# Kernel tuning notes

Measured on AMD Instinct MI355X. Metric: run time of the kernel, lower is better.

The kernel has to match this reference:

```python
import jax, jax.numpy as jnp
import numpy as np

B, H, W, C = 4, 64, 64, 512
EPS = 1e-3  # keras BatchNormalization default epsilon


def setup_inputs() -> dict:
    key = jax.random.key(0)
    ks = jax.random.split(key, 16)
    c8, c2 = C // 8, C // 2
    sc = lambda fan_in: 1.0 / np.sqrt(fan_in)
    inp = {
        "x": jax.random.normal(ks[0], (B, H, W, C), dtype=jnp.float32),
        # 1x1 conv weights as [Cin, Cout] matrices
        "wf": jax.random.normal(ks[1], (C, c8), dtype=jnp.float32) * sc(C),
        "bf": jnp.zeros((c8,), jnp.float32),
        "wg": jax.random.normal(ks[2], (C, c8), dtype=jnp.float32) * sc(C),
        "bg": jnp.zeros((c8,), jnp.float32),
        "wh": jax.random.normal(ks[3], (C, c2), dtype=jnp.float32) * sc(C),
        "bh": jnp.zeros((c2,), jnp.float32),
        "wo": jax.random.normal(ks[4], (c2, C), dtype=jnp.float32) * sc(c2),
        "bo": jnp.zeros((C,), jnp.float32),
        "gamma": jax.random.normal(ks[5], (1,), dtype=jnp.float32) * 0.05,
        # concat 1x1 conv (2C -> C), has bias (use_batchnorm=False default)
        "wc": jax.random.normal(ks[6], (2 * C, C), dtype=jnp.float32) * sc(2 * C),
        "bc": jnp.zeros((C,), jnp.float32),
        # BN inference params (moving statistics)
        "bn_scale": jnp.ones((C,), jnp.float32),
        "bn_bias": jnp.zeros((C,), jnp.float32),
        "bn_mean": jnp.zeros((C,), jnp.float32),
        "bn_var": jnp.ones((C,), jnp.float32),
    }
    return inp


def reference(x, wf, bf, wg, bg, wh, bh, wo, bo, gamma, wc, bc,
              bn_scale, bn_bias, bn_mean, bn_var):
    b, h, w, c = x.shape
    n = h * w
    xf = x.reshape(b, n, c)
    f = xf @ wf + bf          # [B, N, C/8]
    g = xf @ wg + bg          # [B, N, C/8]
    hv = xf @ wh + bh         # [B, N, C/2]
    s = jnp.einsum('bnd,bmd->bnm', g, f)   # [B, N, N]
    beta = jax.nn.softmax(s, axis=-1)
    o = jnp.einsum('bnm,bmd->bnd', beta, hv)  # [B, N, C/2]
    o = o @ wo + bo                            # [B, N, C]
    att = gamma * o + xf                       # gamma-scaled residual
    cat = jnp.concatenate([att, xf], axis=-1)  # [B, N, 2C]
    y = cat @ wc + bc
    # BatchNorm inference + relu
    y = (y - bn_mean) * (bn_scale / jnp.sqrt(bn_var + EPS)) + bn_bias
    y = jax.nn.relu(y)
    return y.reshape(b, h, w, c)
```

## Files before the change

kernel.cpp:

```cpp
#include <hip/hip_runtime.h>
#include <hip/hip_bf16.h>

typedef __bf16 bf16x8 __attribute__((ext_vector_type(8)));
typedef float f32x4 __attribute__((ext_vector_type(4)));

#define EPSBN 1e-3f

constexpr int NPIX = 4096;
constexpr int D2 = 256;

#define RAW_BARRIER() do { \
  asm volatile("s_waitcnt lgkmcnt(0)" ::: "memory"); \
  __builtin_amdgcn_s_barrier(); \
  asm volatile("" ::: "memory"); \
} while (0)

__global__ __launch_bounds__(256) void k_cvt(const float* __restrict__ x,
                                             __bf16* __restrict__ xb, int n4) {
  int i = blockIdx.x * 256 + threadIdx.x;
  if (i >= n4) return;
  float4 v = reinterpret_cast<const float4*>(x)[i];
  union { __bf16 h[4]; uint2 u; } o;
  o.h[0] = (__bf16)v.x; o.h[1] = (__bf16)v.y; o.h[2] = (__bf16)v.z; o.h[3] = (__bf16)v.w;
  reinterpret_cast<uint2*>(xb)[i] = o.u;
}

__global__ __launch_bounds__(256) void kp_wfgh(const float* __restrict__ wf,
                                               const float* __restrict__ wg,
                                               const float* __restrict__ wh,
                                               __bf16* __restrict__ WT) {
  int idx = blockIdx.x * 256 + threadIdx.x;
  int c = idx >> 9, k = idx & 511;
  float v = (c < 64) ? wf[k * 64 + c] : (c < 128) ? wg[k * 64 + (c - 64)] : wh[k * 256 + (c - 128)];
  WT[idx] = (__bf16)v;
}

__global__ __launch_bounds__(128) void kp_bias384(const float* bf_, const float* bg_,
                                                  const float* bh_, float* bias) {
  int c = blockIdx.x * 128 + threadIdx.x;
  bias[c] = (c < 64) ? bf_[c] : (c < 128) ? bg_[c - 64] : bh_[c - 128];
}

__global__ __launch_bounds__(256) void kp_wow(const float* __restrict__ wo,
                                              const float* __restrict__ wc,
                                              float* __restrict__ Wow) {
  int idx = blockIdx.x * 256 + threadIdx.x;
  int d = idx >> 9, c = idx & 511;
  float acc = 0.f;
  for (int j = 0; j < 512; ++j) acc += wo[d * 512 + j] * wc[j * 512 + c];
  Wow[idx] = acc;
}

__global__ __launch_bounds__(256) void kp_wcat(const float* __restrict__ Wow,
                                               const float* __restrict__ wc,
                                               const float* __restrict__ gamma,
                                               const float* __restrict__ bns,
                                               const float* __restrict__ bnv,
                                               __bf16* __restrict__ WT) {
  int idx = blockIdx.x * 256 + threadIdx.x;
  int c = idx / 768, k = idx % 768;
  float s = bns[c] * rsqrtf(bnv[c] + EPSBN);
  float v;
  if (k < 256) v = gamma[0] * Wow[k * 512 + c] * s;
  else { int kk = k - 256; v = (wc[kk * 512 + c] + wc[(512 + kk) * 512 + c]) * s; }
  WT[idx] = (__bf16)v;
}

__global__ __launch_bounds__(256) void kp_biasF(const float* bo, const float* wc, const float* bc,
                                                const float* gamma, const float* bns, const float* bnb,
                                                const float* bnm, const float* bnv, float* biasF) {
  int c = blockIdx.x * 256 + threadIdx.x;
  float s = bns[c] * rsqrtf(bnv[c] + EPSBN);
  float acc = 0.f;
  for (int j = 0; j < 512; ++j) acc += bo[j] * wc[j * 512 + c];
  float pre = bc[c] + gamma[0] * acc;
  biasF[c] = (pre - bnm[c]) * s + bnb[c];
}

template <int KT, int NC, int MODE>
__global__ __launch_bounds__(256) void k_gemm(const __bf16* __restrict__ A1, int k1, int lda1,
                                              const __bf16* __restrict__ A2, int lda2,
                                              const __bf16* __restrict__ WT,
                                              const float* __restrict__ bias,
                                              void* __restrict__ out1,
                                              void* __restrict__ out2) {
  __shared__ __bf16 As[128][72];
  __shared__ __bf16 Ws[64][72];
  const int m0 = blockIdx.x * 128, n0 = blockIdx.y * 64;
  const int tid = threadIdx.x, lane = tid & 63, w = tid >> 6;
  const int wr = w >> 1, wcl = w & 1;
  const int l15 = lane & 15, l4 = lane >> 4;
  f32x4 acc[4][2] = {};
  for (int ks = 0; ks < KT; ks += 64) {
    const __bf16* Asrc; int lda, kb;
    if (ks < k1) { Asrc = A1; lda = lda1; kb = ks; }
    else         { Asrc = A2; lda = lda2; kb = ks - k1; }
#pragma unroll
    for (int it = 0; it < 4; ++it) {
      int idx = it * 256 + tid, r = idx >> 3, ch = idx & 7;
      *(bf16x8*)(&As[r][ch * 8]) = *(const bf16x8*)(Asrc + (size_t)(m0 + r) * lda + kb + ch * 8);
    }
#pragma unroll
    for (int it = 0; it < 2; ++it) {
      int idx = it * 256 + tid, r = idx >> 3, ch = idx & 7;
      *(bf16x8*)(&Ws[r][ch * 8]) = *(const bf16x8*)(WT + (size_t)(n0 + r) * KT + ks + ch * 8);
    }
    __syncthreads();
#pragma unroll
    for (int kk = 0; kk < 2; ++kk) {
      int krd = kk * 32 + l4 * 8;
      bf16x8 av[4], bv[2];
#pragma unroll
      for (int mi = 0; mi < 4; ++mi) av[mi] = *(const bf16x8*)(&As[wr * 64 + mi * 16 + l15][krd]);
#pragma unroll
      for (int ni = 0; ni < 2; ++ni) bv[ni] = *(const bf16x8*)(&Ws[wcl * 32 + ni * 16 + l15][krd]);
#pragma unroll
      for (int mi = 0; mi < 4; ++mi)
#pragma unroll
        for (int ni = 0; ni < 2; ++ni)
          acc[mi][ni] = __builtin_amdgcn_mfma_f32_16x16x32_bf16(av[mi], bv[ni], acc[mi][ni], 0, 0, 0);
    }
    __syncthreads();
  }
#pragma unroll
  for (int mi = 0; mi < 4; ++mi)
#pragma unroll
    for (int ni = 0; ni < 2; ++ni) {
      int col = n0 + wcl * 32 + ni * 16 + l15;
      float bcol = bias[col];
      int row0 = m0 + wr * 64 + mi * 16 + l4 * 4;
      if (MODE == 1) {
        float* out = (float*)out1;
#pragma unroll
        for (int r = 0; r < 4; ++r)
          out[(size_t)(row0 + r) * NC + col] = fmaxf(acc[mi][ni][r] + bcol, 0.f);
      } else {
        if (col < 128) {
          __bf16* fg = (__bf16*)out1;
#pragma unroll
          for (int r = 0; r < 4; ++r)
            fg[(size_t)(row0 + r) * 128 + col] = (__bf16)(acc[mi][ni][r] + bcol);
        } else {
          __bf16* hvT = (__bf16*)out2;
          int bb = row0 >> 12, n = row0 & 4095;
          union { __bf16 h[4]; uint2 u; } pk;
#pragma unroll
          for (int r = 0; r < 4; ++r) pk.h[r] = (__bf16)(acc[mi][ni][r] + bcol);
          *(uint2*)(hvT + ((size_t)(bb * 256 + (col - 128))) * 4096 + n) = pk.u;
        }
      }
    }
}

__global__ __launch_bounds__(512, 2) void k_attn(const __bf16* __restrict__ fg,
                                                 const __bf16* __restrict__ hvT,
                                                 __bf16* __restrict__ obuf) {
  __shared__ __bf16 PsT[2][64][136];
  __shared__ float Lp[8][64];
  const int id = blockIdx.x;
  const int xcd = id & 7, i2 = id >> 3;
  const int b = xcd >> 1;
  const int q0 = (i2 * 2 + (xcd & 1)) * 64;
  const int tid = threadIdx.x, w = tid >> 6, lane = tid & 63;
  const int l15 = lane & 15, l4 = lane >> 4;
  const __bf16* fgb = fg + (size_t)b * NPIX * 128;
  const __bf16* vb = hvT + (size_t)b * D2 * NPIX;

  bf16x8 bG[4][2];
#pragma unroll
  for (int qt = 0; qt < 4; ++qt)
#pragma unroll
    for (int kk = 0; kk < 2; ++kk)
      bG[qt][kk] = *(const bf16x8*)(fgb + (size_t)(q0 + qt * 16 + l15) * 128 + 64 + kk * 32 + l4 * 8);

  bf16x8 aF[2], bV[2][4];
#pragma unroll
  for (int kk = 0; kk < 2; ++kk)
    aF[kk] = *(const bf16x8*)(fgb + (size_t)(w * 16 + l15) * 128 + kk * 32 + l4 * 8);
#pragma unroll
  for (int dj = 0; dj < 2; ++dj)
#pragma unroll
    for (int k4 = 0; k4 < 4; ++k4)
      bV[dj][k4] = *(const bf16x8*)(vb + (size_t)(w * 32 + dj * 16 + l15) * NPIX + k4 * 32 + l4 * 8);

  f32x4 accO[4][2] = {};
  float lsum[4] = {0.f, 0.f, 0.f, 0.f};

  for (int t = 0; t < 32; ++t) {
    const int mn = ((t + 1) * 128) & (NPIX - 1);
    const int bufi = t & 1;
    f32x4 s[4];
#pragma unroll
    for (int qt = 0; qt < 4; ++qt) {
      s[qt] = (f32x4){0.f, 0.f, 0.f, 0.f};
#pragma unroll
      for (int kk = 0; kk < 2; ++kk)
        s[qt] = __builtin_amdgcn_mfma_f32_16x16x32_bf16(aF[kk], bG[qt][kk], s[qt], 0, 0, 0);
    }
    bf16x8 aFn[2];
#pragma unroll
    for (int kk = 0; kk < 2; ++kk)
      aFn[kk] = *(const bf16x8*)(fgb + (size_t)(mn + w * 16 + l15) * 128 + kk * 32 + l4 * 8);
#pragma unroll
    for (int qt = 0; qt < 4; ++qt) {
      float p0 = __expf(s[qt][0]), p1 = __expf(s[qt][1]);
      float p2 = __expf(s[qt][2]), p3 = __expf(s[qt][3]);
      lsum[qt] += (p0 + p1) + (p2 + p3);
      union { __bf16 h[2]; uint u; } w0, w1;
      w0.h[0] = (__bf16)p0; w0.h[1] = (__bf16)p1;
      w1.h[0] = (__bf16)p2; w1.h[1] = (__bf16)p3;
      *(uint*)(&PsT[bufi][qt * 16 + l15][w * 16 + l4 * 4]) = w0.u;
      *(uint*)(&PsT[bufi][qt * 16 + l15][w * 16 + l4 * 4 + 2]) = w1.u;
    }
    RAW_BARRIER();
#pragma unroll
    for (int qt = 0; qt < 4; ++qt) {
      bf16x8 aP[4];
#pragma unroll
      for (int k4 = 0; k4 < 4; ++k4)
        aP[k4] = *(const bf16x8*)(&PsT[bufi][qt * 16 + l15][k4 * 32 + l4 * 8]);
#pragma unroll
      for (int dj = 0; dj < 2; ++dj)
#pragma unroll
        for (int k4 = 0; k4 < 4; ++k4)
          accO[qt][dj] = __builtin_amdgcn_mfma_f32_16x16x32_bf16(aP[k4], bV[dj][k4], accO[qt][dj], 0, 0, 0);
    }
#pragma unroll
    for (int dj = 0; dj < 2; ++dj)
#pragma unroll
      for (int k4 = 0; k4 < 4; ++k4)
        bV[dj][k4] = *(const bf16x8*)(vb + (size_t)(w * 32 + dj * 16 + l15) * NPIX + mn + k4 * 32 + l4 * 8);
    aF[0] = aFn[0]; aF[1] = aFn[1];
  }

#pragma unroll
  for (int qt = 0; qt < 4; ++qt) {
    float v = lsum[qt];
    v += __shfl_xor(v, 16); v += __shfl_xor(v, 32);
    lsum[qt] = v;
  }
  if (l4 == 0) {
#pragma unroll
    for (int qt = 0; qt < 4; ++qt) Lp[w][qt * 16 + l15] = lsum[qt];
  }
  __syncthreads();
  float inv[4][4];
#pragma unroll
  for (int qt = 0; qt < 4; ++qt)
#pragma unroll
    for (int r = 0; r < 4; ++r) {
      int q = qt * 16 + l4 * 4 + r;
      float lt = 0.f;
#pragma unroll
      for (int ww = 0; ww < 8; ++ww) lt += Lp[ww][q];
      inv[qt][r] = 1.0f / lt;
    }
  __bf16* ob = obuf + ((size_t)b * NPIX + q0) * D2;
#pragma unroll
  for (int qt = 0; qt < 4; ++qt)
#pragma unroll
    for (int dj = 0; dj < 2; ++dj)
#pragma unroll
      for (int r = 0; r < 4; ++r)
        ob[(size_t)(qt * 16 + l4 * 4 + r) * D2 + w * 32 + dj * 16 + l15] =
            (__bf16)(accO[qt][dj][r] * inv[qt][r]);
}

extern "C" void kernel_launch(void* const* d_in, const int* in_sizes, int n_in,
                              void* d_out, int out_size, void* d_ws, size_t ws_size,
                              hipStream_t stream) {
  const float* x = (const float*)d_in[0];
  const float* wf = (const float*)d_in[1];
  const float* bf_ = (const float*)d_in[2];
  const float* wg = (const float*)d_in[3];
  const float* bg_ = (const float*)d_in[4];
  const float* wh = (const float*)d_in[5];
  const float* bh_ = (const float*)d_in[6];
  const float* wo = (const float*)d_in[7];
  const float* bo = (const float*)d_in[8];
  const float* gamma = (const float*)d_in[9];
  const float* wc = (const float*)d_in[10];
  const float* bc = (const float*)d_in[11];
  const float* bns = (const float*)d_in[12];
  const float* bnb = (const float*)d_in[13];
  const float* bnm = (const float*)d_in[14];
  const float* bnv = (const float*)d_in[15];
  (void)in_sizes; (void)n_in; (void)out_size; (void)ws_size;

  char* ws = (char*)d_ws;
  __bf16* xb     = (__bf16*)(ws + 0);
  __bf16* fg     = (__bf16*)(ws + 16777216);
  __bf16* hvT    = (__bf16*)(ws + 20971520);
  __bf16* obuf   = (__bf16*)(ws + 29360128);
  __bf16* WfghT  = (__bf16*)(ws + 37748736);
  float*  bias384= (float*) (ws + 38141952);
  float*  Wow    = (float*) (ws + 38143488);
  __bf16* WcatT  = (__bf16*)(ws + 38667776);
  float*  biasF  = (float*) (ws + 39454208);
  float* out = (float*)d_out;

  hipLaunchKernelGGL(k_cvt, dim3(8192), dim3(256), 0, stream, x, xb, 2097152);
  hipLaunchKernelGGL(kp_wfgh, dim3(768), dim3(256), 0, stream, wf, wg, wh, WfghT);
  hipLaunchKernelGGL(kp_bias384, dim3(3), dim3(128), 0, stream, bf_, bg_, bh_, bias384);
  hipLaunchKernelGGL(kp_wow, dim3(512), dim3(256), 0, stream, wo, wc, Wow);
  hipLaunchKernelGGL(kp_wcat, dim3(1536), dim3(256), 0, stream, Wow, wc, gamma, bns, bnv, WcatT);
  hipLaunchKernelGGL(kp_biasF, dim3(2), dim3(256), 0, stream, bo, wc, bc, gamma, bns, bnb, bnm, bnv, biasF);
  hipLaunchKernelGGL((k_gemm<512, 384, 0>), dim3(128, 6), dim3(256), 0, stream,
                     xb, 512, 512, xb, 512, WfghT, bias384, (void*)fg, (void*)hvT);
  hipLaunchKernelGGL(k_attn, dim3(256), dim3(512), 0, stream, fg, hvT, obuf);
  hipLaunchKernelGGL((k_gemm<768, 512, 1>), dim3(128, 8), dim3(256), 0, stream,
                     obuf, 256, 256, xb, 512, WcatT, biasF, (void*)out, nullptr);
}
```

Measured before the change: 278.4 us.

## Split attention keys across blocks and keep probabilities in registers via permlane swaps

Rewrites the attention kernel so each wave handles 32 queries over half of the key range using 32x32x16 MFMAs. The exponentiated scores are packed to bf16 and rearranged across lanes with permlane32_swap to form the PV operand directly, which removes the LDS staging of P and the per-tile barrier. Partial outputs and row sums from the two key halves are written to a workspace and merged by a new combine kernel. In exchange it adds an extra kernel launch and extra global traffic for the partial results. The heavy double-buffered register use at one block per CU reduces occupancy.

```diff
diff --git a/kernel.cpp b/kernel.cpp
--- a/kernel.cpp
+++ b/kernel.cpp
@@ -3,17 +3,13 @@
 
 typedef __bf16 bf16x8 __attribute__((ext_vector_type(8)));
 typedef float f32x4 __attribute__((ext_vector_type(4)));
+typedef float f32x16 __attribute__((ext_vector_type(16)));
+typedef unsigned int uint2v __attribute__((ext_vector_type(2)));
 
 #define EPSBN 1e-3f
 
 constexpr int NPIX = 4096;
 constexpr int D2 = 256;
-
-#define RAW_BARRIER() do { \
-  asm volatile("s_waitcnt lgkmcnt(0)" ::: "memory"); \
-  __builtin_amdgcn_s_barrier(); \
-  asm volatile("" ::: "memory"); \
-} while (0)
 
 __global__ __launch_bounds__(256) void k_cvt(const float* __restrict__ x,
                                              __bf16* __restrict__ xb, int n4) {
@@ -152,118 +148,140 @@
     }
 }
 
-__global__ __launch_bounds__(512, 2) void k_attn(const __bf16* __restrict__ fg,
+
+__device__ __forceinline__ void plswap(unsigned int a, unsigned int b,
+                                       unsigned int& x, unsigned int& y) {
+#if __has_builtin(__builtin_amdgcn_permlane32_swap)
+  uint2v r = __builtin_amdgcn_permlane32_swap(a, b, false, false);
+  x = r.x; y = r.y;
+#else
+  unsigned int as = __shfl_xor((int)a, 32), bs = __shfl_xor((int)b, 32);
+  int hi = (threadIdx.x & 63) >> 5;
+  x = hi ? bs : a;
+  y = hi ? b : as;
+#endif
+}
+
+__global__ __launch_bounds__(256, 1) void k_attn(const __bf16* __restrict__ fg,
                                                  const __bf16* __restrict__ hvT,
-                                                 __bf16* __restrict__ obuf) {
-  __shared__ __bf16 PsT[2][64][136];
-  __shared__ float Lp[8][64];
+                                                 __bf16* __restrict__ PO,
+                                                 float* __restrict__ Lbuf) {
+  __shared__ __bf16 T[4][32][264];
   const int id = blockIdx.x;
-  const int xcd = id & 7, i2 = id >> 3;
-  const int b = xcd >> 1;
-  const int q0 = (i2 * 2 + (xcd & 1)) * 64;
+  const int grp = id & 7;
+  const int b = grp >> 1, ms = grp & 1;
+  const int qb = id >> 3;
   const int tid = threadIdx.x, w = tid >> 6, lane = tid & 63;
-  const int l15 = lane & 15, l4 = lane >> 4;
+  const int l31 = lane & 31, hi = lane >> 5;
+  const int q0w = qb * 128 + w * 32;
+  const int mbase = ms * 2048;
   const __bf16* fgb = fg + (size_t)b * NPIX * 128;
   const __bf16* vb = hvT + (size_t)b * D2 * NPIX;
 
-  bf16x8 bG[4][2];
-#pragma unroll
-  for (int qt = 0; qt < 4; ++qt)
-#pragma unroll
-    for (int kk = 0; kk < 2; ++kk)
-      bG[qt][kk] = *(const bf16x8*)(fgb + (size_t)(q0 + qt * 16 + l15) * 128 + 64 + kk * 32 + l4 * 8);
-
-  bf16x8 aF[2], bV[2][4];
-#pragma unroll
-  for (int kk = 0; kk < 2; ++kk)
-    aF[kk] = *(const bf16x8*)(fgb + (size_t)(w * 16 + l15) * 128 + kk * 32 + l4 * 8);
-#pragma unroll
-  for (int dj = 0; dj < 2; ++dj)
-#pragma unroll
-    for (int k4 = 0; k4 < 4; ++k4)
-      bV[dj][k4] = *(const bf16x8*)(vb + (size_t)(w * 32 + dj * 16 + l15) * NPIX + k4 * 32 + l4 * 8);
-
-  f32x4 accO[4][2] = {};
-  float lsum[4] = {0.f, 0.f, 0.f, 0.f};
-
-  for (int t = 0; t < 32; ++t) {
-    const int mn = ((t + 1) * 128) & (NPIX - 1);
-    const int bufi = t & 1;
-    f32x4 s[4];
-#pragma unroll
-    for (int qt = 0; qt < 4; ++qt) {
-      s[qt] = (f32x4){0.f, 0.f, 0.f, 0.f};
-#pragma unroll
-      for (int kk = 0; kk < 2; ++kk)
-        s[qt] = __builtin_amdgcn_mfma_f32_16x16x32_bf16(aF[kk], bG[qt][kk], s[qt], 0, 0, 0);
-    }
-    bf16x8 aFn[2];
-#pragma unroll
-    for (int kk = 0; kk < 2; ++kk)
-      aFn[kk] = *(const bf16x8*)(fgb + (size_t)(mn + w * 16 + l15) * 128 + kk * 32 + l4 * 8);
-#pragma unroll
-    for (int qt = 0; qt < 4; ++qt) {
-      float p0 = __expf(s[qt][0]), p1 = __expf(s[qt][1]);
-      float p2 = __expf(s[qt][2]), p3 = __expf(s[qt][3]);
-      lsum[qt] += (p0 + p1) + (p2 + p3);
-      union { __bf16 h[2]; uint u; } w0, w1;
-      w0.h[0] = (__bf16)p0; w0.h[1] = (__bf16)p1;
-      w1.h[0] = (__bf16)p2; w1.h[1] = (__bf16)p3;
-      *(uint*)(&PsT[bufi][qt * 16 + l15][w * 16 + l4 * 4]) = w0.u;
-      *(uint*)(&PsT[bufi][qt * 16 + l15][w * 16 + l4 * 4 + 2]) = w1.u;
-    }
-    RAW_BARRIER();
-#pragma unroll
-    for (int qt = 0; qt < 4; ++qt) {
-      bf16x8 aP[4];
-#pragma unroll
-      for (int k4 = 0; k4 < 4; ++k4)
-        aP[k4] = *(const bf16x8*)(&PsT[bufi][qt * 16 + l15][k4 * 32 + l4 * 8]);
-#pragma unroll
-      for (int dj = 0; dj < 2; ++dj)
-#pragma unroll
-        for (int k4 = 0; k4 < 4; ++k4)
-          accO[qt][dj] = __builtin_amdgcn_mfma_f32_16x16x32_bf16(aP[k4], bV[dj][k4], accO[qt][dj], 0, 0, 0);
-    }
-#pragma unroll
-    for (int dj = 0; dj < 2; ++dj)
-#pragma unroll
-      for (int k4 = 0; k4 < 4; ++k4)
-        bV[dj][k4] = *(const bf16x8*)(vb + (size_t)(w * 32 + dj * 16 + l15) * NPIX + mn + k4 * 32 + l4 * 8);
-    aF[0] = aFn[0]; aF[1] = aFn[1];
-  }
-
-#pragma unroll
-  for (int qt = 0; qt < 4; ++qt) {
-    float v = lsum[qt];
-    v += __shfl_xor(v, 16); v += __shfl_xor(v, 32);
-    lsum[qt] = v;
-  }
-  if (l4 == 0) {
-#pragma unroll
-    for (int qt = 0; qt < 4; ++qt) Lp[w][qt * 16 + l15] = lsum[qt];
-  }
-  __syncthreads();
-  float inv[4][4];
-#pragma unroll
-  for (int qt = 0; qt < 4; ++qt)
-#pragma unroll
-    for (int r = 0; r < 4; ++r) {
-      int q = qt * 16 + l4 * 4 + r;
-      float lt = 0.f;
-#pragma unroll
-      for (int ww = 0; ww < 8; ++ww) lt += Lp[ww][q];
-      inv[qt][r] = 1.0f / lt;
-    }
-  __bf16* ob = obuf + ((size_t)b * NPIX + q0) * D2;
-#pragma unroll
-  for (int qt = 0; qt < 4; ++qt)
-#pragma unroll
-    for (int dj = 0; dj < 2; ++dj)
-#pragma unroll
-      for (int r = 0; r < 4; ++r)
-        ob[(size_t)(qt * 16 + l4 * 4 + r) * D2 + w * 32 + dj * 16 + l15] =
-            (__bf16)(accO[qt][dj][r] * inv[qt][r]);
+  bf16x8 bG[4];
+#pragma unroll
+  for (int kt = 0; kt < 4; ++kt)
+    bG[kt] = *(const bf16x8*)(fgb + (size_t)(q0w + l31) * 128 + 64 + kt * 16 + hi * 8);
+
+  f32x16 accO[8] = {};
+  float lsum = 0.f;
+
+  bf16x8 aFA[4], aFB[4], bVA[8][2], bVB[8][2];
+#pragma unroll
+  for (int kt = 0; kt < 4; ++kt)
+    aFA[kt] = *(const bf16x8*)(fgb + (size_t)(mbase + l31) * 128 + kt * 16 + hi * 8);
+#pragma unroll
+  for (int dt = 0; dt < 8; ++dt) {
+    bVA[dt][0] = *(const bf16x8*)(vb + (size_t)(dt * 32 + l31) * NPIX + mbase + hi * 8);
+    bVA[dt][1] = *(const bf16x8*)(vb + (size_t)(dt * 32 + l31) * NPIX + mbase + 16 + hi * 8);
+  }
+
+#define TILE_BODY(MB, MN, AF, AFN, BV, BVN) do {                                        \
+    f32x16 s = {};                                                                      \
+    _Pragma("unroll")                                                                   \
+    for (int kt = 0; kt < 4; ++kt)                                                      \
+      s = __builtin_amdgcn_mfma_f32_32x32x16_bf16(AF[kt], bG[kt], s, 0, 0, 0);          \
+    _Pragma("unroll")                                                                   \
+    for (int kt = 0; kt < 4; ++kt)                                                      \
+      AFN[kt] = *(const bf16x8*)(fgb + (size_t)((MN) + l31) * 128 + kt * 16 + hi * 8);  \
+    _Pragma("unroll")                                                                   \
+    for (int dt = 0; dt < 8; ++dt) {                                                    \
+      BVN[dt][0] = *(const bf16x8*)(vb + (size_t)(dt * 32 + l31) * NPIX + (MN) + hi * 8);        \
+      BVN[dt][1] = *(const bf16x8*)(vb + (size_t)(dt * 32 + l31) * NPIX + (MN) + 16 + hi * 8);   \
+    }                                                                                   \
+    float p[16];                                                                        \
+    _Pragma("unroll")                                                                   \
+    for (int r = 0; r < 16; ++r) p[r] = __expf(s[r]);                                   \
+    lsum += (((p[0] + p[1]) + (p[2] + p[3])) + ((p[4] + p[5]) + (p[6] + p[7]))) +       \
+            (((p[8] + p[9]) + (p[10] + p[11])) + ((p[12] + p[13]) + (p[14] + p[15])));  \
+    unsigned int c01, c23, c45, c67, c89, cAB, cCD, cEF;                                \
+    asm("v_cvt_pk_bf16_f32 %0, %1, %2" : "=v"(c01) : "v"(p[0]), "v"(p[1]));             \
+    asm("v_cvt_pk_bf16_f32 %0, %1, %2" : "=v"(c23) : "v"(p[2]), "v"(p[3]));             \
+    asm("v_cvt_pk_bf16_f32 %0, %1, %2" : "=v"(c45) : "v"(p[4]), "v"(p[5]));             \
+    asm("v_cvt_pk_bf16_f32 %0, %1, %2" : "=v"(c67) : "v"(p[6]), "v"(p[7]));             \
+    asm("v_cvt_pk_bf16_f32 %0, %1, %2" : "=v"(c89) : "v"(p[8]), "v"(p[9]));             \
+    asm("v_cvt_pk_bf16_f32 %0, %1, %2" : "=v"(cAB) : "v"(p[10]), "v"(p[11]));           \
+    asm("v_cvt_pk_bf16_f32 %0, %1, %2" : "=v"(cCD) : "v"(p[12]), "v"(p[13]));           \
+    asm("v_cvt_pk_bf16_f32 %0, %1, %2" : "=v"(cEF) : "v"(p[14]), "v"(p[15]));           \
+    unsigned int f0a, f0c, f0b, f0d, f1a, f1c, f1b, f1d;                                \
+    plswap(c01, c45, f0a, f0b);                                                         \
+    plswap(c23, c67, f0c, f0d);                                                         \
+    plswap(c89, cCD, f1a, f1b);                                                         \
+    plswap(cAB, cEF, f1c, f1d);                                                         \
+    union { unsigned int u[4]; bf16x8 v; } pa0, pa1;                                    \
+    pa0.u[0] = f0a; pa0.u[1] = f0c; pa0.u[2] = f0b; pa0.u[3] = f0d;                     \
+    pa1.u[0] = f1a; pa1.u[1] = f1c; pa1.u[2] = f1b; pa1.u[3] = f1d;                     \
+    _Pragma("unroll")                                                                   \
+    for (int dt = 0; dt < 8; ++dt)                                                      \
+      accO[dt] = __builtin_amdgcn_mfma_f32_32x32x16_bf16(pa0.v, BV[dt][0], accO[dt], 0, 0, 0); \
+    _Pragma("unroll")                                                                   \
+    for (int dt = 0; dt < 8; ++dt)                                                      \
+      accO[dt] = __builtin_amdgcn_mfma_f32_32x32x16_bf16(pa1.v, BV[dt][1], accO[dt], 0, 0, 0); \
+  } while (0)
+
+  for (int tt = 0; tt < 32; ++tt) {
+    const int mb0 = mbase + tt * 64;
+    const int mb1 = mb0 + 32;
+    const int mb2 = mbase + ((tt * 64 + 64) & 2047);
+    TILE_BODY(mb0, mb1, aFA, aFB, bVA, bVB);
+    TILE_BODY(mb1, mb2, aFB, aFA, bVB, bVA);
+  }
+#undef TILE_BODY
+
+  lsum += __shfl_xor(lsum, 32);
+  if (lane < 32)
+    Lbuf[ms * 16384 + b * 4096 + q0w + l31] = lsum;
+
+#pragma unroll
+  for (int dt = 0; dt < 8; ++dt) {
+    int d = dt * 32 + l31;
+#pragma unroll
+    for (int r = 0; r < 16; ++r) {
+      int ql = (r & 3) + 8 * (r >> 2) + 4 * hi;
+      T[w][ql][d] = (__bf16)accO[dt][r];
+    }
+  }
+  __bf16* poB = PO + ((size_t)(ms * 4 + b) * 4096 + q0w) * 256;
+  const int qr = lane >> 1, dh = (lane & 1) * 128;
+#pragma unroll
+  for (int j = 0; j < 16; ++j) {
+    bf16x8 v = *(const bf16x8*)(&T[w][qr][dh + j * 8]);
+    *(bf16x8*)(poB + (size_t)qr * 256 + dh + j * 8) = v;
+  }
+}
+
+__global__ __launch_bounds__(256) void k_comb(const __bf16* __restrict__ PO,
+                                              const float* __restrict__ Lbuf,
+                                              __bf16* __restrict__ obuf) {
+  int idx = blockIdx.x * 256 + threadIdx.x;
+  int row = idx >> 5, d0 = (idx & 31) * 8;
+  float inv = 1.0f / (Lbuf[row] + Lbuf[16384 + row]);
+  bf16x8 a = *(const bf16x8*)(PO + (size_t)row * 256 + d0);
+  bf16x8 c = *(const bf16x8*)(PO + 4194304 + (size_t)row * 256 + d0);
+  bf16x8 o;
+#pragma unroll
+  for (int j = 0; j < 8; ++j) o[j] = (__bf16)(((float)a[j] + (float)c[j]) * inv);
+  *(bf16x8*)(obuf + (size_t)row * 256 + d0) = o;
 }
 
 extern "C" void kernel_launch(void* const* d_in, const int* in_sizes, int n_in,
@@ -291,12 +309,14 @@
   __bf16* xb     = (__bf16*)(ws + 0);
   __bf16* fg     = (__bf16*)(ws + 16777216);
   __bf16* hvT    = (__bf16*)(ws + 20971520);
+  __bf16* PO     = (__bf16*)(ws + 29360128);
   __bf16* obuf   = (__bf16*)(ws + 29360128);
-  __bf16* WfghT  = (__bf16*)(ws + 37748736);
-  float*  bias384= (float*) (ws + 38141952);
-  float*  Wow    = (float*) (ws + 38143488);
-  __bf16* WcatT  = (__bf16*)(ws + 38667776);
-  float*  biasF  = (float*) (ws + 39454208);
+  float*  Lbuf   = (float*) (ws + 46137344);
+  __bf16* WfghT  = (__bf16*)(ws + 46268416);
+  float*  bias384= (float*) (ws + 46661632);
+  float*  Wow    = (float*) (ws + 46663168);
+  __bf16* WcatT  = (__bf16*)(ws + 47187456);
+  float*  biasF  = (float*) (ws + 47973888);
   float* out = (float*)d_out;
 
   hipLaunchKernelGGL(k_cvt, dim3(8192), dim3(256), 0, stream, x, xb, 2097152);
@@ -307,7 +327,8 @@
   hipLaunchKernelGGL(kp_biasF, dim3(2), dim3(256), 0, stream, bo, wc, bc, gamma, bns, bnb, bnm, bnv, biasF);
   hipLaunchKernelGGL((k_gemm<512, 384, 0>), dim3(128, 6), dim3(256), 0, stream,
                      xb, 512, 512, xb, 512, WfghT, bias384, (void*)fg, (void*)hvT);
-  hipLaunchKernelGGL(k_attn, dim3(256), dim3(512), 0, stream, fg, hvT, obuf);
+  hipLaunchKernelGGL(k_attn, dim3(256), dim3(256), 0, stream, fg, hvT, PO, Lbuf);
+  hipLaunchKernelGGL(k_comb, dim3(2048), dim3(256), 0, stream, PO, Lbuf, obuf);
   hipLaunchKernelGGL((k_gemm<768, 512, 1>), dim3(128, 8), dim3(256), 0, stream,
                      obuf, 256, 256, xb, 512, WcatT, biasF, (void*)out, nullptr);
 }
```

Measured after the change: 355.9 us. 27.9% more time.

## Split attention value dimension across two blocks and unroll weight-fold loops

Applied to the files above, without the earlier changes.

The attention kernel now splits the 256-wide value dimension into two halves handled by separate blocks, doubling the grid to 512 blocks and raising the occupancy hint to 4 blocks per CU. Each block keeps only one V fragment set and one output accumulator per query tile, which lowers register pressure. The trade-off is that QK^T and the exp/softmax work are computed twice per query tile. Separately, the weight-folding precompute kernels use four independent accumulators and a vectorized load to shorten their dependency chains.

```diff
diff --git a/kernel.cpp b/kernel.cpp
--- a/kernel.cpp
+++ b/kernel.cpp
@@ -46,9 +46,15 @@
                                               float* __restrict__ Wow) {
   int idx = blockIdx.x * 256 + threadIdx.x;
   int d = idx >> 9, c = idx & 511;
-  float acc = 0.f;
-  for (int j = 0; j < 512; ++j) acc += wo[d * 512 + j] * wc[j * 512 + c];
-  Wow[idx] = acc;
+  float a0 = 0.f, a1 = 0.f, a2 = 0.f, a3 = 0.f;
+  for (int j = 0; j < 512; j += 4) {
+    float4 w4 = *reinterpret_cast<const float4*>(wo + d * 512 + j);
+    a0 += w4.x * wc[(size_t)j * 512 + c];
+    a1 += w4.y * wc[(size_t)(j + 1) * 512 + c];
+    a2 += w4.z * wc[(size_t)(j + 2) * 512 + c];
+    a3 += w4.w * wc[(size_t)(j + 3) * 512 + c];
+  }
+  Wow[idx] = (a0 + a1) + (a2 + a3);
 }
 
 __global__ __launch_bounds__(256) void kp_wcat(const float* __restrict__ Wow,
@@ -71,9 +77,14 @@
                                                 const float* bnm, const float* bnv, float* biasF) {
   int c = blockIdx.x * 256 + threadIdx.x;
   float s = bns[c] * rsqrtf(bnv[c] + EPSBN);
-  float acc = 0.f;
-  for (int j = 0; j < 512; ++j) acc += bo[j] * wc[j * 512 + c];
-  float pre = bc[c] + gamma[0] * acc;
+  float a0 = 0.f, a1 = 0.f, a2 = 0.f, a3 = 0.f;
+  for (int j = 0; j < 512; j += 4) {
+    a0 += bo[j] * wc[(size_t)j * 512 + c];
+    a1 += bo[j + 1] * wc[(size_t)(j + 1) * 512 + c];
+    a2 += bo[j + 2] * wc[(size_t)(j + 2) * 512 + c];
+    a3 += bo[j + 3] * wc[(size_t)(j + 3) * 512 + c];
+  }
+  float pre = bc[c] + gamma[0] * ((a0 + a1) + (a2 + a3));
   biasF[c] = (pre - bnm[c]) * s + bnb[c];
 }
 
@@ -152,7 +163,7 @@
     }
 }
 
-__global__ __launch_bounds__(512, 2) void k_attn(const __bf16* __restrict__ fg,
+__global__ __launch_bounds__(512, 4) void k_attn(const __bf16* __restrict__ fg,
                                                  const __bf16* __restrict__ hvT,
                                                  __bf16* __restrict__ obuf) {
   __shared__ __bf16 PsT[2][64][136];
@@ -160,9 +171,11 @@
   const int id = blockIdx.x;
   const int xcd = id & 7, i2 = id >> 3;
   const int b = xcd >> 1;
-  const int q0 = (i2 * 2 + (xcd & 1)) * 64;
+  const int dh = i2 & 1;
+  const int q0 = ((i2 >> 1) * 2 + (xcd & 1)) * 64;
   const int tid = threadIdx.x, w = tid >> 6, lane = tid & 63;
   const int l15 = lane & 15, l4 = lane >> 4;
+  const int dcol = dh * 128 + w * 16;
   const __bf16* fgb = fg + (size_t)b * NPIX * 128;
   const __bf16* vb = hvT + (size_t)b * D2 * NPIX;
 
@@ -173,17 +186,15 @@
     for (int kk = 0; kk < 2; ++kk)
       bG[qt][kk] = *(const bf16x8*)(fgb + (size_t)(q0 + qt * 16 + l15) * 128 + 64 + kk * 32 + l4 * 8);
 
-  bf16x8 aF[2], bV[2][4];
+  bf16x8 aF[2], bV[4];
 #pragma unroll
   for (int kk = 0; kk < 2; ++kk)
     aF[kk] = *(const bf16x8*)(fgb + (size_t)(w * 16 + l15) * 128 + kk * 32 + l4 * 8);
 #pragma unroll
-  for (int dj = 0; dj < 2; ++dj)
-#pragma unroll
-    for (int k4 = 0; k4 < 4; ++k4)
-      bV[dj][k4] = *(const bf16x8*)(vb + (size_t)(w * 32 + dj * 16 + l15) * NPIX + k4 * 32 + l4 * 8);
-
-  f32x4 accO[4][2] = {};
+  for (int k4 = 0; k4 < 4; ++k4)
+    bV[k4] = *(const bf16x8*)(vb + (size_t)(dcol + l15) * NPIX + k4 * 32 + l4 * 8);
+
+  f32x4 accO[4] = {};
   float lsum[4] = {0.f, 0.f, 0.f, 0.f};
 
   for (int t = 0; t < 32; ++t) {
@@ -220,16 +231,12 @@
       for (int k4 = 0; k4 < 4; ++k4)
         aP[k4] = *(const bf16x8*)(&PsT[bufi][qt * 16 + l15][k4 * 32 + l4 * 8]);
 #pragma unroll
-      for (int dj = 0; dj < 2; ++dj)
-#pragma unroll
-        for (int k4 = 0; k4 < 4; ++k4)
-          accO[qt][dj] = __builtin_amdgcn_mfma_f32_16x16x32_bf16(aP[k4], bV[dj][k4], accO[qt][dj], 0, 0, 0);
-    }
-#pragma unroll
-    for (int dj = 0; dj < 2; ++dj)
-#pragma unroll
       for (int k4 = 0; k4 < 4; ++k4)
-        bV[dj][k4] = *(const bf16x8*)(vb + (size_t)(w * 32 + dj * 16 + l15) * NPIX + mn + k4 * 32 + l4 * 8);
+        accO[qt] = __builtin_amdgcn_mfma_f32_16x16x32_bf16(aP[k4], bV[k4], accO[qt], 0, 0, 0);
+    }
+#pragma unroll
+    for (int k4 = 0; k4 < 4; ++k4)
+      bV[k4] = *(const bf16x8*)(vb + (size_t)(dcol + l15) * NPIX + mn + k4 * 32 + l4 * 8);
     aF[0] = aFn[0]; aF[1] = aFn[1];
   }
 
@@ -259,11 +266,9 @@
 #pragma unroll
   for (int qt = 0; qt < 4; ++qt)
 #pragma unroll
-    for (int dj = 0; dj < 2; ++dj)
-#pragma unroll
-      for (int r = 0; r < 4; ++r)
-        ob[(size_t)(qt * 16 + l4 * 4 + r) * D2 + w * 32 + dj * 16 + l15] =
-            (__bf16)(accO[qt][dj][r] * inv[qt][r]);
+    for (int r = 0; r < 4; ++r)
+      ob[(size_t)(qt * 16 + l4 * 4 + r) * D2 + dcol + l15] =
+          (__bf16)(accO[qt][r] * inv[qt][r]);
 }
 
 extern "C" void kernel_launch(void* const* d_in, const int* in_sizes, int n_in,
@@ -307,7 +312,7 @@
   hipLaunchKernelGGL(kp_biasF, dim3(2), dim3(256), 0, stream, bo, wc, bc, gamma, bns, bnb, bnm, bnv, biasF);
   hipLaunchKernelGGL((k_gemm<512, 384, 0>), dim3(128, 6), dim3(256), 0, stream,
                      xb, 512, 512, xb, 512, WfghT, bias384, (void*)fg, (void*)hvT);
-  hipLaunchKernelGGL(k_attn, dim3(256), dim3(512), 0, stream, fg, hvT, obuf);
+  hipLaunchKernelGGL(k_attn, dim3(512), dim3(512), 0, stream, fg, hvT, obuf);
   hipLaunchKernelGGL((k_gemm<768, 512, 1>), dim3(128, 8), dim3(256), 0, stream,
                      obuf, 256, 256, xb, 512, WcatT, biasF, (void*)out, nullptr);
 }
```

After: 283.6 us. About the same (+1.9%).
